# Performance work log

Measured on AMD Instinct MI355X. Metric: run time of the kernel, lower is better.

The kernel has to match this reference:

```python
import jax, jax.numpy as jnp
import numpy as np

M, N, DIM, BATCH = 64, 64, 256, 4096
GRID = M * N
ALPHA = 0.5
SIGMA = float(np.sqrt(M * N) / 2.0)  # 32.0, default sigma


def _grid_locations():
    ii, jj = np.meshgrid(np.arange(M), np.arange(N), indexing='ij')
    return np.stack([ii.ravel(), jj.ravel()], axis=1).astype(np.int64)  # [GRID, 2]


def _grid_distance_mat(locs):
    # non-periodic: squared euclidean distance between grid locations
    d = locs[:, None, :].astype(np.float32) - locs[None, :, :].astype(np.float32)
    return (d ** 2).sum(-1).astype(np.float32)  # [GRID, GRID]


def setup_inputs() -> dict:
    key = jax.random.key(0)
    k1, k2 = jax.random.split(key)
    locs = _grid_locations()
    return {
        'x': jax.random.normal(k1, (BATCH, DIM), dtype=jnp.float32),
        'centroids': jax.random.normal(k2, (GRID, DIM), dtype=jnp.float32),
        'distance_mat': jnp.asarray(_grid_distance_mat(locs)),
        'locations': jnp.asarray(locs),
        'learning_rate_op': jnp.ones((), dtype=jnp.float32),
    }


def reference(x, centroids, distance_mat, locations, learning_rate_op):
    B = x.shape[0]
    # cdist(x, centroids) with p=2: [B, GRID]
    d2 = ((x ** 2).sum(-1, keepdims=True)
          + (centroids ** 2).sum(-1)[None, :]
          - 2.0 * x @ centroids.T)
    dists = jnp.sqrt(jnp.maximum(d2, 0.0))
    bmu_index = jnp.argmin(dists, axis=-1)            # [B]
    mindist = jnp.min(dists, axis=-1)                 # [B]
    bmu_loc = locations[bmu_index]                    # [B, 2]

    alpha_op = ALPHA * learning_rate_op
    sigma_op = SIGMA * learning_rate_op
    bmu_dist_sq = distance_mat[bmu_index]             # gather rows: [B, GRID]
    neighbourhood = jnp.exp(-bmu_dist_sq / (2.0 * sigma_op ** 2 + 1e-5))
    lrm = alpha_op * neighbourhood                    # [B, GRID]

    # delta = mean_b lrm[b,g] * (x[b,d] - centroids[g,d]), factored to avoid [B,GRID,DIM]
    delta = (lrm.T @ x) / B - jnp.mean(lrm, axis=0)[:, None] * centroids
    new_centroids = centroids + delta
    return new_centroids, bmu_loc, jnp.mean(mindist)
```

## Files before the change

kernel.cpp:

```cpp
#include <hip/hip_runtime.h>
#include <cstdint>
#include <cstddef>

#define DIM    256
#define BATCH  4096
#define STEPS  12

typedef _Float16 f16x8 __attribute__((ext_vector_type(8)));
typedef _Float16 f16x4 __attribute__((ext_vector_type(4)));
typedef float    f32x4 __attribute__((ext_vector_type(4)));

#define OFF_APK  0u
#define OFF_S    0u
#define OFF_BPK  1048576u
#define OFF_CNT  1048576u
#define OFF_U    1052672u
#define OFF_GX   2101248u
#define OFF_WCNT 2105344u
#define OFF_XN   2109440u
#define OFF_CN   2113536u
#define OFF_MD   2117632u
#define OFF_PV   2121728u
#define OFF_PI   2252800u

#define OUT_BMU  1048576u
#define OUT_MD   1056768u

__device__ __forceinline__ void load_lds16(const void* g, void* l) {
  __builtin_amdgcn_global_load_lds(
      (const __attribute__((address_space(1))) unsigned int*)g,
      (__attribute__((address_space(3))) unsigned int*)l, 16, 0, 0);
}

__global__ __launch_bounds__(256) void packnorm_kernel(
    const float* __restrict__ x, const float* __restrict__ cen,
    const float* __restrict__ lr,
    _Float16* __restrict__ Apk, _Float16* __restrict__ Bpk,
    float* __restrict__ xn, float* __restrict__ cn, float* __restrict__ Gx) {
  int row  = blockIdx.x * 4 + (threadIdx.x >> 6);
  int lane = threadIdx.x & 63;
  bool isx = row < BATCH;
  const float* src = isx ? (x + (size_t)row * DIM)
                         : (cen + (size_t)(row - BATCH) * DIM);
  float4 v = *(const float4*)(src + lane * 4);
  _Float16 h0 = (_Float16)v.x, h1 = (_Float16)v.y,
           h2 = (_Float16)v.z, h3 = (_Float16)v.w;
  _Float16 l0 = (_Float16)(v.x - (float)h0), l1 = (_Float16)(v.y - (float)h1),
           l2 = (_Float16)(v.z - (float)h2), l3 = (_Float16)(v.w - (float)h3);
  _Float16* dst = (isx ? Apk : Bpk) + (size_t)(isx ? row : row - BATCH) * 512;
  *(f16x4*)(dst + lane * 4)       = (f16x4){h0, h1, h2, h3};
  *(f16x4*)(dst + 256 + lane * 4) = (f16x4){l0, l1, l2, l3};
  float s = v.x * v.x + v.y * v.y + v.z * v.z + v.w * v.w;
#pragma unroll
  for (int off = 32; off >= 1; off >>= 1) s += __shfl_xor(s, off);
  if (lane == 0) { if (isx) xn[row] = s; else cn[row - BATCH] = s; }
  if (blockIdx.x == 0) {
    float sg  = 32.f * lr[0];
    float inv = 1.f / (2.f * sg * sg + 1e-5f);
#pragma unroll
    for (int i = 0; i < 16; ++i) {
      int g = i * 256 + threadIdx.x;
      float d = (float)((g >> 6) - (g & 63));
      Gx[g] = expf(-d * d * inv);
    }
  }
}

__global__ __launch_bounds__(256) void gemm_argmin_kernel(
    const _Float16* __restrict__ Apk, const _Float16* __restrict__ Bpk,
    const float* __restrict__ cnorm, float* __restrict__ pv, int* __restrict__ pi) {
  __shared__ __align__(16) _Float16 lds[2][8192];
  const int tid  = threadIdx.x;
  const int lane = tid & 63, w = tid >> 6;
  const int wr = w >> 1, wc = w & 1;
  const int row0 = blockIdx.y * 128, col0 = blockIdx.x * 128;
  const int t15 = lane & 15, q = lane >> 4;
  const int sw  = t15 & 7;
  const int srow   = w * 32 + (lane >> 3);
  const int schunk = (lane & 7) ^ ((lane >> 3) & 7);

  f32x4 acc[4][4];
#pragma unroll
  for (int m = 0; m < 4; ++m)
#pragma unroll
    for (int n = 0; n < 4; ++n) acc[m][n] = (f32x4){0.f, 0.f, 0.f, 0.f};

  for (int t = 0; t < STEPS; ++t) {
    if (t) __syncthreads();
    {
      const int seg = t >> 2, k = (t & 3) << 6;
      const int aoff = ((seg == 2) ? 256 : 0) + k;
      const int boff = ((seg == 1) ? 256 : 0) + k;
      const _Float16* Ab = Apk + (size_t)(row0 + srow) * 512 + aoff + schunk * 8;
      const _Float16* Bb = Bpk + (size_t)(col0 + srow) * 512 + boff + schunk * 8;
      _Float16* Al = &lds[0][w * 2048];
      _Float16* Bl = &lds[1][w * 2048];
#pragma unroll
      for (int i = 0; i < 4; ++i) {
        load_lds16(Ab + (size_t)i * 8 * 512, Al + i * 512);
        load_lds16(Bb + (size_t)i * 8 * 512, Bl + i * 512);
      }
    }
    __syncthreads();
#pragma unroll
    for (int kk = 0; kk < 2; ++kk) {
      f16x8 af[4], bf[4];
#pragma unroll
      for (int m = 0; m < 4; ++m) {
        int r = wr * 64 + m * 16 + t15;
        af[m] = *(const f16x8*)&lds[0][r * 64 + (((kk * 4 + q) ^ sw) * 8)];
      }
#pragma unroll
      for (int n = 0; n < 4; ++n) {
        int r = wc * 64 + n * 16 + t15;
        bf[n] = *(const f16x8*)&lds[1][r * 64 + (((kk * 4 + q) ^ sw) * 8)];
      }
#pragma unroll
      for (int m = 0; m < 4; ++m)
#pragma unroll
        for (int n = 0; n < 4; ++n)
          acc[m][n] = __builtin_amdgcn_mfma_f32_16x16x32_f16(af[m], bf[n], acc[m][n], 0, 0, 0);
    }
  }
  __syncthreads();

  float cnv[4];
#pragma unroll
  for (int n = 0; n < 4; ++n) cnv[n] = cnorm[col0 + wc * 64 + n * 16 + t15];

  float* cv = (float*)&lds[0][0];
  int*   ci = (int*)&lds[1][0];
#pragma unroll
  for (int m = 0; m < 4; ++m) {
#pragma unroll
    for (int reg = 0; reg < 4; ++reg) {
      float bv = 1e30f; int bi = 0x7fffffff;
#pragma unroll
      for (int n = 0; n < 4; ++n) {
        float v = cnv[n] - 2.f * acc[m][n][reg];
        if (v < bv) { bv = v; bi = col0 + wc * 64 + n * 16 + t15; }
      }
#pragma unroll
      for (int off = 1; off < 16; off <<= 1) {
        float ov = __shfl_xor(bv, off);
        int   oi = __shfl_xor(bi, off);
        if (ov < bv || (ov == bv && oi < bi)) { bv = ov; bi = oi; }
      }
      if (t15 == 0) {
        int r = wr * 64 + m * 16 + q * 4 + reg;
        cv[r * 2 + wc] = bv;
        ci[r * 2 + wc] = bi;
      }
    }
  }
  __syncthreads();
  if (tid < 128) {
    float v0 = cv[tid * 2];     int i0 = ci[tid * 2];
    float v1 = cv[tid * 2 + 1]; int i1 = ci[tid * 2 + 1];
    if (v1 < v0 || (v1 == v0 && i1 < i0)) { v0 = v1; i0 = i1; }
    pv[(size_t)(row0 + tid) * 32 + blockIdx.x] = v0;
    pi[(size_t)(row0 + tid) * 32 + blockIdx.x] = i0;
  }
}

__global__ __launch_bounds__(256) void finalize_kernel(
    const float* __restrict__ pv, const int* __restrict__ pi,
    const float* __restrict__ xn, const float* __restrict__ x,
    float* __restrict__ S, float* __restrict__ cnt,
    float* __restrict__ md, float* __restrict__ out) {
  const int w = threadIdx.x >> 6, l = threadIdx.x & 63;
  const int b = blockIdx.x * 4 + w;
  float v = pv[(size_t)b * 32 + (l & 31)];
  int idx  = pi[(size_t)b * 32 + (l & 31)];
#pragma unroll
  for (int off = 16; off >= 1; off >>= 1) {
    float ov = __shfl_xor(v, off);
    int   oi = __shfl_xor(idx, off);
    if (ov < v || (ov == v && oi < idx)) { v = ov; idx = oi; }
  }
  if (l == 0) {
    md[b] = sqrtf(fmaxf(xn[b] + v, 0.f));
    out[OUT_BMU + (size_t)b * 2 + 0] = (float)(idx >> 6);
    out[OUT_BMU + (size_t)b * 2 + 1] = (float)(idx & 63);
    atomicAdd(cnt + idx, 1.f);
  }
#pragma unroll
  for (int c = 0; c < 4; ++c)
    atomicAdd(S + (size_t)idx * DIM + c * 64 + l, x[(size_t)b * DIM + c * 64 + l]);
}

__global__ __launch_bounds__(256) void e1_kernel(const float* __restrict__ S,
                                                 const float* __restrict__ Gx,
                                                 const float* __restrict__ cnt,
                                                 const float* __restrict__ md,
                                                 float* __restrict__ U,
                                                 float* __restrict__ Wcnt,
                                                 float* __restrict__ out) {
  __shared__ float smem[12288];
  const int bid = blockIdx.x, tid = threadIdx.x;
  if (bid < 256) {
    float* Ss = smem;
    const int dd = tid & 63, gq = tid >> 6;
    const int kj = bid >> 2, dq = bid & 3;
#pragma unroll 4
    for (int i = 0; i < 16; ++i) {
      int ki = i * 4 + gq;
      Ss[ki * 64 + dd] = S[((size_t)ki * 64 + kj) * 256 + dq * 64 + dd];
    }
    __syncthreads();
    float a[16];
#pragma unroll
    for (int gg = 0; gg < 16; ++gg) a[gg] = 0.f;
    for (int ki = 0; ki < 64; ++ki) {
      float s = Ss[ki * 64 + dd];
#pragma unroll
      for (int gg = 0; gg < 16; ++gg)
        a[gg] += Gx[ki * 64 + gq * 16 + gg] * s;
    }
#pragma unroll
    for (int gg = 0; gg < 16; ++gg)
      U[((size_t)(gq * 16 + gg) * 64 + kj) * 256 + dq * 64 + dd] = a[gg];
  } else if (bid < 272) {
    float* cs = smem;
    float* gs = smem + 4096;
    float* inner = smem + 8192;
    for (int i = 0; i < 16; i++) { cs[i * 256 + tid] = cnt[i * 256 + tid]; gs[i * 256 + tid] = Gx[i * 256 + tid]; }
    __syncthreads();
    for (int i = 0; i < 16; i++) {
      int idx = i * 256 + tid; int ki = idx >> 6, gj = idx & 63;
      float a = 0.f;
      for (int kj = 0; kj < 64; kj++) a += gs[kj * 64 + gj] * cs[ki * 64 + kj];
      inner[idx] = a;
    }
    __syncthreads();
    const int g = (bid - 256) * 256 + tid, gi = g >> 6, gj = g & 63;
    float a = 0.f;
    for (int ki = 0; ki < 64; ki++) a += gs[gi * 64 + ki] * inner[ki * 64 + gj];
    Wcnt[g] = a;
  } else {
    float s = 0.f;
#pragma unroll
    for (int i = 0; i < 16; i++) s += md[i * 256 + tid];
#pragma unroll
    for (int off = 32; off >= 1; off >>= 1) s += __shfl_xor(s, off);
    if ((tid & 63) == 0) smem[tid >> 6] = s;
    __syncthreads();
    if (tid == 0) out[OUT_MD] = (smem[0] + smem[1] + smem[2] + smem[3]) * (1.f / (float)BATCH);
  }
}

__global__ __launch_bounds__(256) void e2_kernel(const float* __restrict__ U,
                                                 const float* __restrict__ Gx,
                                                 const float* __restrict__ Wcnt,
                                                 const float* __restrict__ cen,
                                                 const float* __restrict__ lr,
                                                 float* __restrict__ out) {
  __shared__ float Us[4096];
  const int t = threadIdx.x, dd = t & 63, gq = t >> 6;
  const int gi = blockIdx.x >> 2, dq = blockIdx.x & 3;
#pragma unroll 4
  for (int i = 0; i < 16; ++i) {
    int kj = i * 4 + gq;
    Us[kj * 64 + dd] = U[((size_t)gi * 64 + kj) * 256 + dq * 64 + dd];
  }
  __syncthreads();
  float a[16];
#pragma unroll
  for (int gg = 0; gg < 16; ++gg) a[gg] = 0.f;
  for (int kj = 0; kj < 64; ++kj) {
    float s = Us[kj * 64 + dd];
#pragma unroll
    for (int gg = 0; gg < 16; ++gg)
      a[gg] += Gx[kj * 64 + gq * 16 + gg] * s;
  }
  const float coef = 0.5f * lr[0] / (float)BATCH;
#pragma unroll
  for (int gg = 0; gg < 16; ++gg) {
    int g = gi * 64 + gq * 16 + gg;
    float c = cen[(size_t)g * 256 + dq * 64 + dd];
    out[(size_t)g * 256 + dq * 64 + dd] = c + coef * (a[gg] - Wcnt[g] * c);
  }
}

extern "C" void kernel_launch(void* const* d_in, const int* in_sizes, int n_in,
                              void* d_out, int out_size, void* d_ws, size_t ws_size,
                              hipStream_t stream) {
  const float* x   = (const float*)d_in[0];
  const float* cen = (const float*)d_in[1];
  const float* lr  = (const float*)d_in[4];
  float* out = (float*)d_out;
  float* ws  = (float*)d_ws;

  _Float16* Apk = (_Float16*)(ws + OFF_APK);
  _Float16* Bpk = (_Float16*)(ws + OFF_BPK);
  float* S    = ws + OFF_S;
  float* cnt  = ws + OFF_CNT;
  float* U    = ws + OFF_U;
  float* Gx   = ws + OFF_GX;
  float* Wcnt = ws + OFF_WCNT;
  float* xn   = ws + OFF_XN;
  float* cnw  = ws + OFF_CN;
  float* md   = ws + OFF_MD;
  float* pv   = ws + OFF_PV;
  int*   pi   = (int*)(ws + OFF_PI);

  packnorm_kernel<<<2048, 256, 0, stream>>>(x, cen, lr, Apk, Bpk, xn, cnw, Gx);
  gemm_argmin_kernel<<<dim3(32, 32), 256, 0, stream>>>(Apk, Bpk, cnw, pv, pi);
  hipMemsetAsync(S, 0, (size_t)(1048576 + 4096) * sizeof(float), stream);
  finalize_kernel<<<1024, 256, 0, stream>>>(pv, pi, xn, x, S, cnt, md, out);
  e1_kernel<<<273, 256, 0, stream>>>(S, Gx, cnt, md, U, Wcnt, out);
  e2_kernel<<<256, 256, 0, stream>>>(U, Gx, Wcnt, cen, lr, out);
}
```

Measured before the change: 181.1 us.

## Double-buffer LDS staging and interleave hi/lo split-fp16 MFMA per k-step

The split-precision GEMM loop (hi*hi, hi*lo, lo*hi segments) is restructured. Each k-step of 32 now loads the hi and lo halves of both A and B into LDS, with each wave staging one of the four operand planes. The LDS is double-buffered so the next step's global-to-LDS copy overlaps the current step's MFMAs, which drops one barrier per step. LDS use doubles to 64 KB, which may reduce occupancy, and the swizzle changes to a 4-chunk XOR pattern for the narrower 32-element rows.

```diff
diff --git a/kernel.cpp b/kernel.cpp
--- a/kernel.cpp
+++ b/kernel.cpp
@@ -4,7 +4,7 @@
 
 #define DIM    256
 #define BATCH  4096
-#define STEPS  12
+#define KSTEPS 8
 
 typedef _Float16 f16x8 __attribute__((ext_vector_type(8)));
 typedef _Float16 f16x4 __attribute__((ext_vector_type(4)));
@@ -69,15 +69,18 @@
 __global__ __launch_bounds__(256) void gemm_argmin_kernel(
     const _Float16* __restrict__ Apk, const _Float16* __restrict__ Bpk,
     const float* __restrict__ cnorm, float* __restrict__ pv, int* __restrict__ pi) {
-  __shared__ __align__(16) _Float16 lds[2][8192];
+  __shared__ __align__(16) _Float16 lds[2][4][4096];
   const int tid  = threadIdx.x;
   const int lane = tid & 63, w = tid >> 6;
   const int wr = w >> 1, wc = w & 1;
   const int row0 = blockIdx.y * 128, col0 = blockIdx.x * 128;
   const int t15 = lane & 15, q = lane >> 4;
-  const int sw  = t15 & 7;
-  const int srow   = w * 32 + (lane >> 3);
-  const int schunk = (lane & 7) ^ ((lane >> 3) & 7);
+  const int rsw = t15 & 3;
+  const int srow   = lane >> 2;
+  const int schunk = (lane & 3) ^ ((lane >> 2) & 3);
+  const _Float16* sbase = (w < 2) ? (Apk + (size_t)row0 * 512)
+                                  : (Bpk + (size_t)col0 * 512);
+  const int shalf = (w & 1) ? 256 : 0;
 
   f32x4 acc[4][4];
 #pragma unroll
@@ -85,42 +88,42 @@
 #pragma unroll
     for (int n = 0; n < 4; ++n) acc[m][n] = (f32x4){0.f, 0.f, 0.f, 0.f};
 
-  for (int t = 0; t < STEPS; ++t) {
-    if (t) __syncthreads();
-    {
-      const int seg = t >> 2, k = (t & 3) << 6;
-      const int aoff = ((seg == 2) ? 256 : 0) + k;
-      const int boff = ((seg == 1) ? 256 : 0) + k;
-      const _Float16* Ab = Apk + (size_t)(row0 + srow) * 512 + aoff + schunk * 8;
-      const _Float16* Bb = Bpk + (size_t)(col0 + srow) * 512 + boff + schunk * 8;
-      _Float16* Al = &lds[0][w * 2048];
-      _Float16* Bl = &lds[1][w * 2048];
-#pragma unroll
-      for (int i = 0; i < 4; ++i) {
-        load_lds16(Ab + (size_t)i * 8 * 512, Al + i * 512);
-        load_lds16(Bb + (size_t)i * 8 * 512, Bl + i * 512);
+  auto STAGE = [&](int b, int step) {
+    const _Float16* s0 = sbase + shalf + step * 32 + schunk * 8;
+    _Float16* dst = &lds[b][w][0];
+#pragma unroll
+    for (int i = 0; i < 8; ++i)
+      load_lds16(s0 + (size_t)(i * 16 + srow) * 512, dst + i * 512);
+  };
+
+  STAGE(0, 0);
+  for (int t = 0; t < KSTEPS; ++t) {
+    const int b = t & 1;
+    __syncthreads();
+    if (t + 1 < KSTEPS) STAGE(b ^ 1, t + 1);
+    f16x8 afh[4], afl[4], bfh[4], bfl[4];
+#pragma unroll
+    for (int m = 0; m < 4; ++m) {
+      int r = wr * 64 + m * 16 + t15;
+      int c = (q ^ rsw) * 8;
+      afh[m] = *(const f16x8*)&lds[b][0][r * 32 + c];
+      afl[m] = *(const f16x8*)&lds[b][1][r * 32 + c];
+    }
+#pragma unroll
+    for (int n = 0; n < 4; ++n) {
+      int r = wc * 64 + n * 16 + t15;
+      int c = (q ^ rsw) * 8;
+      bfh[n] = *(const f16x8*)&lds[b][2][r * 32 + c];
+      bfl[n] = *(const f16x8*)&lds[b][3][r * 32 + c];
+    }
+#pragma unroll
+    for (int m = 0; m < 4; ++m)
+#pragma unroll
+      for (int n = 0; n < 4; ++n) {
+        acc[m][n] = __builtin_amdgcn_mfma_f32_16x16x32_f16(afh[m], bfh[n], acc[m][n], 0, 0, 0);
+        acc[m][n] = __builtin_amdgcn_mfma_f32_16x16x32_f16(afh[m], bfl[n], acc[m][n], 0, 0, 0);
+        acc[m][n] = __builtin_amdgcn_mfma_f32_16x16x32_f16(afl[m], bfh[n], acc[m][n], 0, 0, 0);
       }
-    }
-    __syncthreads();
-#pragma unroll
-    for (int kk = 0; kk < 2; ++kk) {
-      f16x8 af[4], bf[4];
-#pragma unroll
-      for (int m = 0; m < 4; ++m) {
-        int r = wr * 64 + m * 16 + t15;
-        af[m] = *(const f16x8*)&lds[0][r * 64 + (((kk * 4 + q) ^ sw) * 8)];
-      }
-#pragma unroll
-      for (int n = 0; n < 4; ++n) {
-        int r = wc * 64 + n * 16 + t15;
-        bf[n] = *(const f16x8*)&lds[1][r * 64 + (((kk * 4 + q) ^ sw) * 8)];
-      }
-#pragma unroll
-      for (int m = 0; m < 4; ++m)
-#pragma unroll
-        for (int n = 0; n < 4; ++n)
-          acc[m][n] = __builtin_amdgcn_mfma_f32_16x16x32_f16(af[m], bf[n], acc[m][n], 0, 0, 0);
-    }
   }
   __syncthreads();
 
@@ -128,8 +131,8 @@
 #pragma unroll
   for (int n = 0; n < 4; ++n) cnv[n] = cnorm[col0 + wc * 64 + n * 16 + t15];
 
-  float* cv = (float*)&lds[0][0];
-  int*   ci = (int*)&lds[1][0];
+  float* cv = (float*)&lds[0][0][0];
+  int*   ci = (int*)&lds[0][2][0];
 #pragma unroll
   for (int m = 0; m < 4; ++m) {
 #pragma unroll
```

New measurement: 180.7 us. No clear change (-0.2%).
